# Performance work log

Measured on AMD Instinct MI355X. Metric: run time of the kernel, lower is better.

## Reference

```python
import jax, jax.numpy as jnp
import numpy as np
import math

D_MODEL = 512
PATCH_LENS = (8, 16, 32)
MAX_P = 32
TAU = 0.5


def _sinusoid_pe(num_pos, d_model):
    pos = jnp.arange(num_pos, dtype=jnp.float32)[:, None]
    div = jnp.exp(jnp.arange(0, d_model, 2, dtype=jnp.float32) * (-(math.log(10000.0) / d_model)))
    pe = jnp.zeros((num_pos, d_model), dtype=jnp.float32)
    pe = pe.at[:, 0::2].set(jnp.sin(pos * div))
    pe = pe.at[:, 1::2].set(jnp.cos(pos * div))
    return pe  # [num_pos, d_model]


def setup_inputs() -> dict:
    key = jax.random.key(0)
    ks = jax.random.split(key, 10)
    B, C, L = 32, 64, 512
    BC, R, n_exp = B * C, L // MAX_P, len(PATCH_LENS)
    x = jax.random.normal(ks[0], (B, C, L), dtype=jnp.float32)
    u = jax.random.uniform(ks[1], (BC, R, n_exp), dtype=jnp.float32, minval=1e-6, maxval=1.0 - 1e-6)
    gumbel = -jnp.log(-jnp.log(u))
    # router MLP: Linear(max_patch_len, 64) -> ReLU -> Linear(64, n_exp)
    s1 = 1.0 / math.sqrt(MAX_P)
    s2 = 1.0 / math.sqrt(64)
    cls_w1 = jax.random.uniform(ks[2], (MAX_P, 64), jnp.float32, -s1, s1)
    cls_b1 = jax.random.uniform(ks[3], (64,), jnp.float32, -s1, s1)
    cls_w2 = jax.random.uniform(ks[4], (64, n_exp), jnp.float32, -s2, s2)
    cls_b2 = jax.random.uniform(ks[5], (n_exp,), jnp.float32, -s2, s2)
    # per-patch-length expert embeddings: Linear(p, d_model, bias=False)
    emb_w8 = jax.random.uniform(ks[6], (8, D_MODEL), jnp.float32, -1 / math.sqrt(8), 1 / math.sqrt(8))
    emb_w16 = jax.random.uniform(ks[7], (16, D_MODEL), jnp.float32, -1 / math.sqrt(16), 1 / math.sqrt(16))
    emb_w32 = jax.random.uniform(ks[8], (32, D_MODEL), jnp.float32, -1 / math.sqrt(32), 1 / math.sqrt(32))
    return {"x": x, "gumbel": gumbel, "cls_w1": cls_w1, "cls_b1": cls_b1,
            "cls_w2": cls_w2, "cls_b2": cls_b2,
            "emb_w8": emb_w8, "emb_w16": emb_w16, "emb_w32": emb_w32}


def reference(x, gumbel, cls_w1, cls_b1, cls_w2, cls_b2, emb_w8, emb_w16, emb_w32):
    B, C, L = x.shape
    R = L // MAX_P                    # regions per series
    T = MAX_P // min(PATCH_LENS)      # target patches per region (mode='fixed')
    n_exp = len(PATCH_LENS)
    xr = x.reshape(B * C, R, MAX_P)   # [BC, R, P]

    # router MLP per region (vectorized over all regions)
    h = jax.nn.relu(jnp.einsum('brp,pk->brk', xr, cls_w1) + cls_b1)
    logits = jnp.einsum('brk,kn->brn', h, cls_w2) + cls_b2   # [BC, R, n_exp]

    # gumbel-softmax (tau=0.5, hard=True, straight-through)
    y_soft = jax.nn.softmax((logits + gumbel) / TAU, axis=-1)
    idx = jnp.argmax(y_soft, axis=-1)                         # [BC, R]
    y_hard = jax.nn.one_hot(idx, n_exp, dtype=y_soft.dtype)
    cls_soft = y_hard - jax.lax.stop_gradient(y_soft) + y_soft
    cls_pred = jnp.argmax(cls_soft, axis=-1)                  # [BC, R]

    # multi-branch expert embeddings, aligned to T patches via repeat_interleave+truncate
    expert_ws = (emb_w8, emb_w16, emb_w32)
    embs = []
    for p, w in zip(PATCH_LENS, expert_ws):
        n_p = MAX_P // p
        patches = xr.reshape(B * C, R, n_p, p)               # unfold(-1, p, p)
        rep = T - n_p + 1                                     # repeat_interleave factor
        sel = jnp.arange(T) // rep                            # truncated interleave indices
        patches = patches[:, :, sel, :]                       # [BC, R, T, p]
        embs.append(jnp.einsum('brtp,pd->brtd', patches, w))  # [BC, R, T, d]
    stack = jnp.stack(embs, axis=0)                           # [n_exp, BC, R, T, d]

    gates = jnp.transpose(cls_soft, (2, 0, 1))[..., None, None]  # [n_exp, BC, R, 1, 1]
    region_emb = (stack * gates).sum(axis=0)                  # [BC, R, T, d]

    x_patch = region_emb.reshape(B * C, R * T, D_MODEL)
    x_patch = x_patch + _sinusoid_pe(R * T, D_MODEL)[None]

    all_cls_pred = cls_pred.T.reshape(-1)                     # cat over regions along dim 0
    return x_patch, all_cls_pred
```

## Files before the change

kernel.cpp:

```cpp
#include <hip/hip_runtime.h>
#include <hip/hip_bf16.h>

#define DM 512
#define BCN 2048
#define XPATCH ((size_t)BCN * 64 * DM)

__device__ __forceinline__ unsigned pack_bf16(float a, float b) {
    __hip_bfloat162 h = __float22bfloat162_rn(make_float2(a, b));
    return *reinterpret_cast<unsigned*>(&h);
}
__device__ __forceinline__ float2 unpack_bf16(unsigned p) {
    float2 r;
    r.x = __uint_as_float(p << 16);
    r.y = __uint_as_float(p & 0xffff0000u);
    return r;
}
__device__ __forceinline__ void fma4p(float4& a, float xv, float2 wa, float2 wb) {
    a.x = fmaf(xv, wa.x, a.x);
    a.y = fmaf(xv, wa.y, a.y);
    a.z = fmaf(xv, wb.x, a.z);
    a.w = fmaf(xv, wb.y, a.w);
}
__device__ __forceinline__ void fma4f(float4& a, float xv, float4 w) {
    a.x = fmaf(xv, w.x, a.x);
    a.y = fmaf(xv, w.y, a.y);
    a.z = fmaf(xv, w.z, a.z);
    a.w = fmaf(xv, w.w, a.w);
}

__global__ __launch_bounds__(256, 4) void ape_fused(
    const float* __restrict__ x,
    const float* __restrict__ gumbel,
    const float* __restrict__ w1,
    const float* __restrict__ b1,
    const float* __restrict__ w2,
    const float* __restrict__ b2,
    const float* __restrict__ w8,
    const float* __restrict__ w16,
    const float* __restrict__ w32,
    float* __restrict__ out)
{
    __shared__ unsigned w32s[32 * 256];
    __shared__ float    xs[DM];
    __shared__ int      eidx[16];

    const int bc  = blockIdx.x;
    const int tid = threadIdx.x;

    if (tid < 128)
        reinterpret_cast<float4*>(xs)[tid] =
            reinterpret_cast<const float4*>(x + (size_t)bc * DM)[tid];

    #pragma unroll
    for (int it = 0; it < 16; ++it) {
        int f4   = it * 256 + tid;
        int row  = f4 >> 7;
        int col4 = f4 & 127;
        float4 v = reinterpret_cast<const float4*>(w32 + (size_t)row * DM)[col4];
        reinterpret_cast<uint2*>(w32s)[row * 128 + col4] =
            make_uint2(pack_bf16(v.x, v.y), pack_bf16(v.z, v.w));
    }
    __syncthreads();

    {
        const int lane = tid & 63;
        const int wv   = tid >> 6;
        float w1r[32];
        #pragma unroll
        for (int q = 0; q < 32; ++q) w1r[q] = w1[q * 64 + lane];
        const float w2r0 = w2[lane * 3 + 0];
        const float w2r1 = w2[lane * 3 + 1];
        const float w2r2 = w2[lane * 3 + 2];
        const float b1r  = b1[lane];

        #pragma unroll
        for (int p = 0; p < 4; ++p) {
            const int rr = p * 4 + wv;
            const float* xr = xs + rr * 32;
            float a = b1r;
            #pragma unroll
            for (int q = 0; q < 32; ++q) a = fmaf(xr[q], w1r[q], a);
            float h = fmaxf(a, 0.f);
            float p0 = h * w2r0, p1 = h * w2r1, p2 = h * w2r2;
            #pragma unroll
            for (int off = 32; off; off >>= 1) {
                p0 += __shfl_down(p0, off, 64);
                p1 += __shfl_down(p1, off, 64);
                p2 += __shfl_down(p2, off, 64);
            }
            if (lane == 0) {
                const float* g = gumbel + ((size_t)bc * 16 + rr) * 3;
                float s0 = p0 + b2[0] + g[0];
                float s1 = p1 + b2[1] + g[1];
                float s2 = p2 + b2[2] + g[2];
                int best = 0; float bs = s0;
                if (s1 > bs) { bs = s1; best = 1; }
                if (s2 > bs) { best = 2; }
                eidx[rr] = best;
                out[XPATCH + (size_t)rr * BCN + bc] = (float)best;
            }
        }
    }
    __syncthreads();

    const int rp = tid >> 7;
    const int cg = tid & 127;
    const int c0 = cg * 4;
    const float kln = -9.210340371976184f / 256.0f;
    const float dv0 = __expf((float)(cg * 2)     * kln);
    const float dv1 = __expf((float)(cg * 2 + 1) * kln);
    const uint2*  w32b = reinterpret_cast<const uint2*>(w32s) + cg;
    const float4* w8b  = reinterpret_cast<const float4*>(w8)  + cg;
    const float4* w16b = reinterpret_cast<const float4*>(w16) + cg;

    #pragma unroll 1
    for (int p = 0; p < 8; ++p) {
        const int rr = p * 2 + rp;
        const int e  = eidx[rr];
        const int xo = rr * 32;
        float4 a0 = {0,0,0,0}, a1 = {0,0,0,0}, a2 = {0,0,0,0}, a3 = {0,0,0,0};

        if (e == 0) {
            #pragma unroll
            for (int q = 0; q < 8; ++q) {
                float4 wv = w8b[q * 128];
                fma4f(a0, xs[xo + q],      wv);
                fma4f(a1, xs[xo + 8  + q], wv);
                fma4f(a2, xs[xo + 16 + q], wv);
                fma4f(a3, xs[xo + 24 + q], wv);
            }
        } else if (e == 1) {
            #pragma unroll
            for (int q = 0; q < 16; ++q) {
                float4 wv = w16b[q * 128];
                fma4f(a0, xs[xo + q],      wv);
                fma4f(a3, xs[xo + 16 + q], wv);
            }
            a1 = a0; a2 = a0;
        } else {
            #pragma unroll
            for (int q = 0; q < 32; ++q) {
                uint2 pk = w32b[q * 128];
                float2 wa = unpack_bf16(pk.x), wb = unpack_bf16(pk.y);
                fma4p(a0, xs[xo + q], wa, wb);
            }
            a1 = a0; a2 = a0; a3 = a0;
        }

        const size_t ob = ((size_t)(bc * 64 + rr * 4)) * DM + c0;
        float4 av[4] = {a0, a1, a2, a3};
        #pragma unroll
        for (int t = 0; t < 4; ++t) {
            float sv0, cv0, sv1, cv1;
            const float pos = (float)(rr * 4 + t);
            __sincosf(pos * dv0, &sv0, &cv0);
            __sincosf(pos * dv1, &sv1, &cv1);
            float4 o;
            o.x = av[t].x + sv0;
            o.y = av[t].y + cv0;
            o.z = av[t].z + sv1;
            o.w = av[t].w + cv1;
            *reinterpret_cast<float4*>(out + ob + (size_t)t * DM) = o;
        }
    }
}

extern "C" void kernel_launch(void* const* d_in, const int* in_sizes, int n_in,
                              void* d_out, int out_size, void* d_ws, size_t ws_size,
                              hipStream_t stream) {
    const float* x      = (const float*)d_in[0];
    const float* gumbel = (const float*)d_in[1];
    const float* w1     = (const float*)d_in[2];
    const float* b1     = (const float*)d_in[3];
    const float* w2     = (const float*)d_in[4];
    const float* b2     = (const float*)d_in[5];
    const float* w8     = (const float*)d_in[6];
    const float* w16    = (const float*)d_in[7];
    const float* w32    = (const float*)d_in[8];
    float* out = (float*)d_out;

    ape_fused<<<BCN, 256, 0, stream>>>(x, gumbel, w1, b1, w2, b2, w8, w16, w32, out);
}
```

Measured before the change: 295.4 us.

## Compute router per wave redundantly, drop barrier, use nontemporal stores

Each wave now computes the router decision for the 8 regions it will later embed, using xor-shuffle all-reduce so every lane has the result. The decisions are packed into a wave-uniform bitmask, which removes the shared eidx array and the second __syncthreads. The large output writes and the x load switch to nontemporal builtins to avoid cache pollution from streaming data. In exchange, the router MLP work is duplicated across wave pairs (8 regions per wave instead of 4).

```diff
diff --git a/kernel.cpp b/kernel.cpp
--- a/kernel.cpp
+++ b/kernel.cpp
@@ -4,6 +4,8 @@
 #define DM 512
 #define BCN 2048
 #define XPATCH ((size_t)BCN * 64 * DM)
+
+typedef float f32x4 __attribute__((ext_vector_type(4)));
 
 __device__ __forceinline__ unsigned pack_bf16(float a, float b) {
     __hip_bfloat162 h = __float22bfloat162_rn(make_float2(a, b));
@@ -15,13 +17,13 @@
     r.y = __uint_as_float(p & 0xffff0000u);
     return r;
 }
-__device__ __forceinline__ void fma4p(float4& a, float xv, float2 wa, float2 wb) {
+__device__ __forceinline__ void fma4p(f32x4& a, float xv, float2 wa, float2 wb) {
     a.x = fmaf(xv, wa.x, a.x);
     a.y = fmaf(xv, wa.y, a.y);
     a.z = fmaf(xv, wb.x, a.z);
     a.w = fmaf(xv, wb.y, a.w);
 }
-__device__ __forceinline__ void fma4f(float4& a, float xv, float4 w) {
+__device__ __forceinline__ void fma4f(f32x4& a, float xv, f32x4 w) {
     a.x = fmaf(xv, w.x, a.x);
     a.y = fmaf(xv, w.y, a.y);
     a.z = fmaf(xv, w.z, a.z);
@@ -42,29 +44,34 @@
 {
     __shared__ unsigned w32s[32 * 256];
     __shared__ float    xs[DM];
-    __shared__ int      eidx[16];
 
     const int bc  = blockIdx.x;
     const int tid = threadIdx.x;
 
-    if (tid < 128)
-        reinterpret_cast<float4*>(xs)[tid] =
-            reinterpret_cast<const float4*>(x + (size_t)bc * DM)[tid];
+    if (tid < 128) {
+        f32x4 v = __builtin_nontemporal_load(
+            reinterpret_cast<const f32x4*>(x + (size_t)bc * DM) + tid);
+        reinterpret_cast<f32x4*>(xs)[tid] = v;
+    }
 
     #pragma unroll
     for (int it = 0; it < 16; ++it) {
         int f4   = it * 256 + tid;
         int row  = f4 >> 7;
         int col4 = f4 & 127;
-        float4 v = reinterpret_cast<const float4*>(w32 + (size_t)row * DM)[col4];
+        f32x4 v = reinterpret_cast<const f32x4*>(w32 + (size_t)row * DM)[col4];
         reinterpret_cast<uint2*>(w32s)[row * 128 + col4] =
             make_uint2(pack_bf16(v.x, v.y), pack_bf16(v.z, v.w));
     }
     __syncthreads();
 
+    const int lane = tid & 63;
+    const int wv   = tid >> 6;
+    const int pw   = wv & 1;
+    const int ch   = wv >> 1;
+
+    unsigned epack = 0;
     {
-        const int lane = tid & 63;
-        const int wv   = tid >> 6;
         float w1r[32];
         #pragma unroll
         for (int q = 0; q < 32; ++q) w1r[q] = w1[q * 64 + lane];
@@ -72,10 +79,11 @@
         const float w2r1 = w2[lane * 3 + 1];
         const float w2r2 = w2[lane * 3 + 2];
         const float b1r  = b1[lane];
+        const float b20  = b2[0], b21 = b2[1], b22 = b2[2];
 
         #pragma unroll
-        for (int p = 0; p < 4; ++p) {
-            const int rr = p * 4 + wv;
+        for (int p = 0; p < 8; ++p) {
+            const int rr = p * 2 + pw;
             const float* xr = xs + rr * 32;
             float a = b1r;
             #pragma unroll
@@ -83,58 +91,57 @@
             float h = fmaxf(a, 0.f);
             float p0 = h * w2r0, p1 = h * w2r1, p2 = h * w2r2;
             #pragma unroll
-            for (int off = 32; off; off >>= 1) {
-                p0 += __shfl_down(p0, off, 64);
-                p1 += __shfl_down(p1, off, 64);
-                p2 += __shfl_down(p2, off, 64);
+            for (int off = 1; off < 64; off <<= 1) {
+                p0 += __shfl_xor(p0, off, 64);
+                p1 += __shfl_xor(p1, off, 64);
+                p2 += __shfl_xor(p2, off, 64);
             }
-            if (lane == 0) {
-                const float* g = gumbel + ((size_t)bc * 16 + rr) * 3;
-                float s0 = p0 + b2[0] + g[0];
-                float s1 = p1 + b2[1] + g[1];
-                float s2 = p2 + b2[2] + g[2];
-                int best = 0; float bs = s0;
-                if (s1 > bs) { bs = s1; best = 1; }
-                if (s2 > bs) { best = 2; }
-                eidx[rr] = best;
-                out[XPATCH + (size_t)rr * BCN + bc] = (float)best;
-            }
+            const float* g = gumbel + ((size_t)bc * 16 + rr) * 3;
+            float s0 = p0 + b20 + g[0];
+            float s1 = p1 + b21 + g[1];
+            float s2 = p2 + b22 + g[2];
+            int best = 0; float bs = s0;
+            if (s1 > bs) { bs = s1; best = 1; }
+            if (s2 > bs) { best = 2; }
+            epack |= (unsigned)best << (2 * p);
+            if ((ch | lane) == 0)
+                __builtin_nontemporal_store(
+                    (float)best, out + XPATCH + (size_t)rr * BCN + bc);
         }
+        epack = (unsigned)__builtin_amdgcn_readfirstlane((int)epack);
     }
-    __syncthreads();
 
-    const int rp = tid >> 7;
-    const int cg = tid & 127;
+    const int cg = ch * 64 + lane;
     const int c0 = cg * 4;
     const float kln = -9.210340371976184f / 256.0f;
     const float dv0 = __expf((float)(cg * 2)     * kln);
     const float dv1 = __expf((float)(cg * 2 + 1) * kln);
     const uint2*  w32b = reinterpret_cast<const uint2*>(w32s) + cg;
-    const float4* w8b  = reinterpret_cast<const float4*>(w8)  + cg;
-    const float4* w16b = reinterpret_cast<const float4*>(w16) + cg;
+    const f32x4*  w8b  = reinterpret_cast<const f32x4*>(w8)  + cg;
+    const f32x4*  w16b = reinterpret_cast<const f32x4*>(w16) + cg;
 
     #pragma unroll 1
     for (int p = 0; p < 8; ++p) {
-        const int rr = p * 2 + rp;
-        const int e  = eidx[rr];
+        const int rr = p * 2 + pw;
+        const int e  = (int)((epack >> (2 * p)) & 3u);
         const int xo = rr * 32;
-        float4 a0 = {0,0,0,0}, a1 = {0,0,0,0}, a2 = {0,0,0,0}, a3 = {0,0,0,0};
+        f32x4 a0 = {0,0,0,0}, a1 = {0,0,0,0}, a2 = {0,0,0,0}, a3 = {0,0,0,0};
 
         if (e == 0) {
             #pragma unroll
             for (int q = 0; q < 8; ++q) {
-                float4 wv = w8b[q * 128];
-                fma4f(a0, xs[xo + q],      wv);
-                fma4f(a1, xs[xo + 8  + q], wv);
-                fma4f(a2, xs[xo + 16 + q], wv);
-                fma4f(a3, xs[xo + 24 + q], wv);
+                f32x4 wvv = w8b[q * 128];
+                fma4f(a0, xs[xo + q],      wvv);
+                fma4f(a1, xs[xo + 8  + q], wvv);
+                fma4f(a2, xs[xo + 16 + q], wvv);
+                fma4f(a3, xs[xo + 24 + q], wvv);
             }
         } else if (e == 1) {
             #pragma unroll
             for (int q = 0; q < 16; ++q) {
-                float4 wv = w16b[q * 128];
-                fma4f(a0, xs[xo + q],      wv);
-                fma4f(a3, xs[xo + 16 + q], wv);
+                f32x4 wvv = w16b[q * 128];
+                fma4f(a0, xs[xo + q],      wvv);
+                fma4f(a3, xs[xo + 16 + q], wvv);
             }
             a1 = a0; a2 = a0;
         } else {
@@ -148,19 +155,20 @@
         }
 
         const size_t ob = ((size_t)(bc * 64 + rr * 4)) * DM + c0;
-        float4 av[4] = {a0, a1, a2, a3};
+        f32x4 av[4] = {a0, a1, a2, a3};
         #pragma unroll
         for (int t = 0; t < 4; ++t) {
             float sv0, cv0, sv1, cv1;
             const float pos = (float)(rr * 4 + t);
             __sincosf(pos * dv0, &sv0, &cv0);
             __sincosf(pos * dv1, &sv1, &cv1);
-            float4 o;
+            f32x4 o;
             o.x = av[t].x + sv0;
             o.y = av[t].y + cv0;
             o.z = av[t].z + sv1;
             o.w = av[t].w + cv1;
-            *reinterpret_cast<float4*>(out + ob + (size_t)t * DM) = o;
+            __builtin_nontemporal_store(
+                o, reinterpret_cast<f32x4*>(out + ob + (size_t)t * DM));
         }
     }
 }
```

New measurement: 375.6 us. 1.27x slower.
